# Kernel optimization log

Measured on AMD Instinct MI355X. Metric: run time of the kernel, lower is better.

The kernel has to match this reference:

```python
import jax, jax.numpy as jnp
import numpy as np

HIDDEN = 768
NUM_HEADS = 12
HEAD_SIZE = HIDDEN // NUM_HEADS
LN_EPS = 1e-5


def setup_inputs() -> dict:
    key = jax.random.key(0)
    ks = jax.random.split(key, 10)
    B, S, H = 2, 4096, HIDDEN
    std = 1.0 / np.sqrt(H)
    inp = {
        "hidden_states": jax.random.normal(ks[0], (B, S, H), dtype=jnp.float32),
        "attention_mask": jnp.ones((B, S), dtype=jnp.float32),
        "Wq": jax.random.normal(ks[1], (H, H), dtype=jnp.float32) * std,
        "bq": jnp.zeros((H,), dtype=jnp.float32),
        "Wk": jax.random.normal(ks[2], (H, H), dtype=jnp.float32) * std,
        "bk": jnp.zeros((H,), dtype=jnp.float32),
        "Wv": jax.random.normal(ks[3], (H, H), dtype=jnp.float32) * std,
        "bv": jnp.zeros((H,), dtype=jnp.float32),
        "Wo": jax.random.normal(ks[4], (H, H), dtype=jnp.float32) * std,
        "bo": jnp.zeros((H,), dtype=jnp.float32),
        "ln_gamma": jnp.ones((H,), dtype=jnp.float32),
        "ln_beta": jnp.zeros((H,), dtype=jnp.float32),
    }
    return inp


def _split_heads(x):
    # [B, S, H] -> [B, nH, S, hd]
    B, S, _ = x.shape
    return x.reshape(B, S, NUM_HEADS, HEAD_SIZE).transpose(0, 2, 1, 3)


def reference(hidden_states, attention_mask, Wq, bq, Wk, bk, Wv, bv, Wo, bo, ln_gamma, ln_beta):
    # QKV projections (torch Linear: x @ W.T + b; here W is stored as [in, out])
    q = _split_heads(hidden_states @ Wq + bq)
    k = _split_heads(hidden_states @ Wk + bk)
    v = _split_heads(hidden_states @ Wv + bv)

    scores = jnp.einsum("bhqd,bhkd->bhqk", q, k) / jnp.sqrt(jnp.float32(HEAD_SIZE))
    # additive mask: (1 - mask) * -10000, broadcast over heads and query positions
    scores = scores + (1.0 - attention_mask)[:, None, None, :] * -10000.0
    probs = jax.nn.softmax(scores, axis=-1)  # dropout_prob = 0 -> identity

    ctx = jnp.einsum("bhqk,bhkd->bhqd", probs, v)
    B, _, S, _ = ctx.shape
    ctx = ctx.transpose(0, 2, 1, 3).reshape(B, S, HIDDEN)

    out = ctx @ Wo + bo
    resid = out + hidden_states
    mu = jnp.mean(resid, axis=-1, keepdims=True)
    var = jnp.var(resid, axis=-1, keepdims=True)
    return (resid - mu) * jax.lax.rsqrt(var + LN_EPS) * ln_gamma + ln_beta
```

## Files before the change

### kernel.cpp

```cpp
#include <hip/hip_runtime.h>
#include <hip/hip_bf16.h>

#define HID 768
#define NHEADS 12
#define HDIM 64
#define SEQ 4096
#define BB 2
#define MTOT (BB * SEQ)

typedef __attribute__((ext_vector_type(8))) short bf16x8;
typedef __attribute__((ext_vector_type(16))) float f32x16;

#define LOG2E 1.4426950408889634f

__device__ inline unsigned pack2bf(float a, float b) {
    __hip_bfloat162 h = __float22bfloat162_rn(float2{a, b});
    return *(unsigned*)&h;
}

__global__ __launch_bounds__(256) void cast_x_kernel(
    const float* __restrict__ X, __hip_bfloat16* __restrict__ Xb)
{
    const size_t i = ((size_t)blockIdx.x * 256 + threadIdx.x) * 8;
    const float4 x0 = *(const float4*)(X + i);
    const float4 x1 = *(const float4*)(X + i + 4);
    unsigned u[4];
    u[0] = pack2bf(x0.x, x0.y);
    u[1] = pack2bf(x0.z, x0.w);
    u[2] = pack2bf(x1.x, x1.y);
    u[3] = pack2bf(x1.z, x1.w);
    *(uint4*)(Xb + i) = *(uint4*)u;
}

__global__ __launch_bounds__(256) void pack_w_kernel(
    const float* __restrict__ Wq, const float* __restrict__ Wk,
    const float* __restrict__ Wv, const float* __restrict__ Wo,
    __hip_bfloat16* __restrict__ Wt)
{
    const int z = blockIdx.z;
    const float* __restrict__ W = (z == 0) ? Wq : (z == 1) ? Wk : (z == 2) ? Wv : Wo;
    const int in0  = blockIdx.x * 64;
    const int out0 = blockIdx.y * 64;
    const int t = threadIdx.x;

    __shared__ float T[64][65];
#pragma unroll
    for (int i = 0; i < 4; ++i) {
        const int idx = t + 256 * i;
        const int row = idx >> 4;
        const int c4  = (idx & 15) << 2;
        const float4 v = *(const float4*)(W + (size_t)(in0 + row) * HID + out0 + c4);
        T[row][c4 + 0] = v.x; T[row][c4 + 1] = v.y;
        T[row][c4 + 2] = v.z; T[row][c4 + 3] = v.w;
    }
    __syncthreads();

    const int o  = t >> 2;
    const int cb = (t & 3) << 4;
    __hip_bfloat16 tmp[16];
#pragma unroll
    for (int k = 0; k < 16; ++k)
        tmp[k] = __float2bfloat16(T[cb + k][o]);
    __hip_bfloat16* __restrict__ dst =
        Wt + (size_t)(z * HID + out0 + o) * HID + in0 + cb;
    *(uint4*)(dst)     = *(uint4*)(&tmp[0]);
    *(uint4*)(dst + 8) = *(uint4*)(&tmp[8]);
}

#define GSTAGE(ASB, BSB, BUF, APTR, BPTR, K0) do {                                 \
    _Pragma("unroll")                                                              \
    for (int j_ = 0; j_ < 4; ++j_) {                                               \
        const __hip_bfloat16* ga_ = (APTR) + (size_t)(r0 + 32 * j_) * HID + (K0) + csw; \
        const __hip_bfloat16* gb_ = (BPTR) + (size_t)(r0 + 32 * j_) * HID + (K0) + csw; \
        __builtin_amdgcn_global_load_lds(                                          \
            (const __attribute__((address_space(1))) unsigned*)ga_,                \
            (__attribute__((address_space(3))) unsigned*)(&ASB[BUF][0][0] + (256 * j_ + 64 * w) * 8), 16, 0, 0); \
        __builtin_amdgcn_global_load_lds(                                          \
            (const __attribute__((address_space(1))) unsigned*)gb_,                \
            (__attribute__((address_space(3))) unsigned*)(&BSB[BUF][0][0] + (256 * j_ + 64 * w) * 8), 16, 0, 0); \
    }                                                                              \
} while (0)

#define GTILE(ASB, BSB, BUF) do {                                                  \
    _Pragma("unroll")                                                              \
    for (int kh = 0; kh < 4; ++kh) {                                               \
        const int sc = ((2 * kh + g) ^ (col & 7)) << 3;                            \
        const bf16x8 a0 = *(const bf16x8*)&ASB[BUF][64 * wm + col][sc];            \
        const bf16x8 a1 = *(const bf16x8*)&ASB[BUF][64 * wm + 32 + col][sc];       \
        const bf16x8 b0 = *(const bf16x8*)&BSB[BUF][64 * wn + col][sc];            \
        const bf16x8 b1 = *(const bf16x8*)&BSB[BUF][64 * wn + 32 + col][sc];       \
        acc[0][0] = __builtin_amdgcn_mfma_f32_32x32x16_bf16(a0, b0, acc[0][0], 0, 0, 0); \
        acc[0][1] = __builtin_amdgcn_mfma_f32_32x32x16_bf16(a0, b1, acc[0][1], 0, 0, 0); \
        acc[1][0] = __builtin_amdgcn_mfma_f32_32x32x16_bf16(a1, b0, acc[1][0], 0, 0, 0); \
        acc[1][1] = __builtin_amdgcn_mfma_f32_32x32x16_bf16(a1, b1, acc[1][1], 0, 0, 0); \
    }                                                                              \
} while (0)

__global__ __launch_bounds__(256) void qkv_mfma_kernel(
    const __hip_bfloat16* __restrict__ Xb, const __hip_bfloat16* __restrict__ Wt,
    const float* __restrict__ bq, const float* __restrict__ bk,
    const float* __restrict__ bv,
    __hip_bfloat16* __restrict__ Qo, __hip_bfloat16* __restrict__ Ko,
    __hip_bfloat16* __restrict__ Vo)
{
    const int nblk = blockIdx.x;
    const int z  = nblk / 6;
    const int f0 = (nblk % 6) * 128;
    const int n0 = nblk * 128;
    const int m0 = blockIdx.y * 128;

    const float* __restrict__ bias = (z == 0) ? bq : (z == 1) ? bk : bv;

    const int t    = threadIdx.x;
    const int w    = t >> 6;
    const int lane = t & 63;
    const int col  = lane & 31;
    const int g    = lane >> 5;
    const int wm   = w & 1;
    const int wn   = w >> 1;

    __shared__ __hip_bfloat16 smem[4 * 128 * 64];
    __hip_bfloat16 (*Asb)[128][64] = (__hip_bfloat16(*)[128][64])smem;
    __hip_bfloat16 (*Bsb)[128][64] = (__hip_bfloat16(*)[128][64])(smem + 2 * 128 * 64);

    const int r0  = t >> 3;
    const int csw = (((t & 7) ^ (r0 & 7)) << 3);

    const __hip_bfloat16* __restrict__ Am = Xb + (size_t)m0 * HID;
    const __hip_bfloat16* __restrict__ Bn = Wt + (size_t)n0 * HID;

    f32x16 acc[2][2];
#pragma unroll
    for (int mt = 0; mt < 2; ++mt)
#pragma unroll
        for (int nt = 0; nt < 2; ++nt)
#pragma unroll
            for (int r = 0; r < 16; ++r) acc[mt][nt][r] = 0.f;

    GSTAGE(Asb, Bsb, 0, Am, Bn, 0);
    __syncthreads();
    for (int k0 = 0; k0 < HID; k0 += 128) {
        GSTAGE(Asb, Bsb, 1, Am, Bn, k0 + 64);
        GTILE(Asb, Bsb, 0);
        __syncthreads();
        if (k0 + 128 < HID) GSTAGE(Asb, Bsb, 0, Am, Bn, k0 + 128);
        GTILE(Asb, Bsb, 1);
        __syncthreads();
    }

    if (z < 2) {
        __hip_bfloat16* __restrict__ Out = (z == 0) ? Qo : Ko;
        const int h = (f0 >> 6) + wn;
#pragma unroll
        for (int mt = 0; mt < 2; ++mt)
#pragma unroll
            for (int nt = 0; nt < 2; ++nt) {
                const int d = 32 * nt + col;
                const float bsv = bias[f0 + 64 * wn + d];
#pragma unroll
                for (int r = 0; r < 16; ++r) {
                    const int m = m0 + 64 * wm + 32 * mt + (r & 3) + 8 * (r >> 2) + 4 * g;
                    const int b = m >> 12;
                    const int s = m & (SEQ - 1);
                    Out[(((size_t)(b * NHEADS + h)) * SEQ + s) * HDIM + d] =
                        __float2bfloat16(acc[mt][nt][r] + bsv);
                }
            }
    } else {
        __syncthreads();
        __hip_bfloat16 (*Ts)[136] = (__hip_bfloat16(*)[136])smem;
#pragma unroll
        for (int mt = 0; mt < 2; ++mt)
#pragma unroll
            for (int nt = 0; nt < 2; ++nt) {
                const int nloc = 64 * wn + 32 * nt + col;
                const float bsv = bias[f0 + nloc];
#pragma unroll
                for (int rg = 0; rg < 4; ++rg) {
                    const int mbase = 64 * wm + 32 * mt + 8 * rg + 4 * g;
                    unsigned pu[2];
                    pu[0] = pack2bf(acc[mt][nt][4 * rg + 0] + bsv,
                                    acc[mt][nt][4 * rg + 1] + bsv);
                    pu[1] = pack2bf(acc[mt][nt][4 * rg + 2] + bsv,
                                    acc[mt][nt][4 * rg + 3] + bsv);
                    *(uint2*)&Ts[nloc][mbase] = *(uint2*)pu;
                }
            }
        __syncthreads();
        const int nloc = t >> 1;
        const int half = t & 1;
        const int hh = (f0 >> 6) + (nloc >> 6);
        const int d  = nloc & 63;
        const int bb = m0 >> 12;
        const int s0 = m0 & (SEQ - 1);
        __hip_bfloat16* __restrict__ dst =
            Vo + (((size_t)(bb * NHEADS + hh)) * HDIM + d) * SEQ + s0 + 64 * half;
        const __hip_bfloat16* srcp = &Ts[nloc][64 * half];
#pragma unroll
        for (int j = 0; j < 8; ++j)
            *(uint4*)(dst + 8 * j) = *(const uint4*)(srcp + 8 * j);
    }
}

typedef __attribute__((ext_vector_type(2))) unsigned uswap2;

__global__ __launch_bounds__(256, 3) void attn_kernel(
    const __hip_bfloat16* __restrict__ Qb, const __hip_bfloat16* __restrict__ Kb,
    const __hip_bfloat16* __restrict__ Vt, const float* __restrict__ mask,
    __hip_bfloat16* __restrict__ Op, float* __restrict__ lp)
{
    const int bh = blockIdx.y;
    const int b  = bh / NHEADS;
    const int h  = bh - b * NHEADS;
    const int kspan = SEQ / gridDim.z;
    const int kbeg  = blockIdx.z * kspan;

    const int t    = threadIdx.x;
    const int w    = t >> 6;
    const int lane = t & 63;
    const int col  = lane & 31;
    const int g    = lane >> 5;
    const int qw   = blockIdx.x * 128 + 32 * w;

    __shared__ __hip_bfloat16 Ksb[2][64][64];
    __shared__ __hip_bfloat16 Vsb[2][64][64];
    __shared__ float madd[2048];

    const __hip_bfloat16* __restrict__ Qh = Qb + (size_t)bh * SEQ * HDIM;
    const __hip_bfloat16* __restrict__ Kh = Kb + (size_t)bh * SEQ * HDIM;
    const __hip_bfloat16* __restrict__ Vh = Vt + (size_t)bh * HDIM * SEQ;

    for (int j = t; j < kspan; j += 256)
        madd[j] = (1.0f - mask[b * SEQ + kbeg + j]) * (-10000.0f * LOG2E);

    const int r0  = t >> 3;
    const int csw = (((t & 7) ^ (r0 & 7)) << 3);

#define STAGE(BUF, KT) do {                                                        \
    const __hip_bfloat16* gk0_ = Kh + (size_t)((KT) + r0) * HDIM + csw;            \
    const __hip_bfloat16* gk1_ = Kh + (size_t)((KT) + r0 + 32) * HDIM + csw;       \
    const __hip_bfloat16* gv0_ = Vh + (size_t)r0 * SEQ + (KT) + csw;               \
    const __hip_bfloat16* gv1_ = Vh + (size_t)(r0 + 32) * SEQ + (KT) + csw;        \
    __hip_bfloat16* lk_ = &Ksb[BUF][0][0] + w * 512;                               \
    __hip_bfloat16* lv_ = &Vsb[BUF][0][0] + w * 512;                               \
    __builtin_amdgcn_global_load_lds(                                              \
        (const __attribute__((address_space(1))) unsigned*)gk0_,                   \
        (__attribute__((address_space(3))) unsigned*)lk_, 16, 0, 0);               \
    __builtin_amdgcn_global_load_lds(                                              \
        (const __attribute__((address_space(1))) unsigned*)gk1_,                   \
        (__attribute__((address_space(3))) unsigned*)(lk_ + 2048), 16, 0, 0);      \
    __builtin_amdgcn_global_load_lds(                                              \
        (const __attribute__((address_space(1))) unsigned*)gv0_,                   \
        (__attribute__((address_space(3))) unsigned*)lv_, 16, 0, 0);               \
    __builtin_amdgcn_global_load_lds(                                              \
        (const __attribute__((address_space(1))) unsigned*)gv1_,                   \
        (__attribute__((address_space(3))) unsigned*)(lv_ + 2048), 16, 0, 0);      \
} while (0)

    bf16x8 bq[4];
#pragma unroll
    for (int kh = 0; kh < 4; ++kh)
        bq[kh] = *(const bf16x8*)(Qh + (size_t)(qw + col) * HDIM + 16 * kh + 8 * g);

    f32x16 O[2];
    float lac = 0.f;
#pragma unroll
    for (int dt = 0; dt < 2; ++dt)
#pragma unroll
        for (int r = 0; r < 16; ++r) O[dt][r] = 0.f;

    const float kscale = 0.125f * LOG2E;

#define ATTN_TILE(BUF, KT0) do {                                                   \
    f32x16 St[2];                                                                  \
    _Pragma("unroll")                                                              \
    for (int nt = 0; nt < 2; ++nt)                                                 \
        _Pragma("unroll")                                                          \
        for (int r = 0; r < 16; ++r) St[nt][r] = 0.f;                              \
    _Pragma("unroll")                                                              \
    for (int kh = 0; kh < 4; ++kh) {                                               \
        const int sc = ((2 * kh + g) ^ (col & 7)) << 3;                            \
        const bf16x8 ak0 = *(const bf16x8*)&Ksb[BUF][col][sc];                     \
        const bf16x8 ak1 = *(const bf16x8*)&Ksb[BUF][32 + col][sc];                \
        St[0] = __builtin_amdgcn_mfma_f32_32x32x16_bf16(ak0, bq[kh], St[0], 0, 0, 0); \
        St[1] = __builtin_amdgcn_mfma_f32_32x32x16_bf16(ak1, bq[kh], St[1], 0, 0, 0); \
    }                                                                              \
    unsigned g4x[2][4], g4y[2][4];                                                 \
    _Pragma("unroll")                                                              \
    for (int nt = 0; nt < 2; ++nt) {                                               \
        _Pragma("unroll")                                                          \
        for (int b4 = 0; b4 < 4; ++b4) {                                           \
            const float4 mm = *(const float4*)&madd[(KT0) + 32 * nt + 8 * b4 + 4 * g]; \
            const float p0 = __builtin_amdgcn_exp2f(fmaf(St[nt][4 * b4 + 0], kscale, mm.x)); \
            const float p1 = __builtin_amdgcn_exp2f(fmaf(St[nt][4 * b4 + 1], kscale, mm.y)); \
            const float p2 = __builtin_amdgcn_exp2f(fmaf(St[nt][4 * b4 + 2], kscale, mm.z)); \
            const float p3 = __builtin_amdgcn_exp2f(fmaf(St[nt][4 * b4 + 3], kscale, mm.w)); \
            lac += (p0 + p1) + (p2 + p3);                                          \
            g4x[nt][b4] = pack2bf(p0, p1);                                         \
            g4y[nt][b4] = pack2bf(p2, p3);                                         \
        }                                                                          \
    }                                                                              \
    _Pragma("unroll")                                                              \
    for (int kh = 0; kh < 4; ++kh) {                                               \
        const int nt  = kh >> 1;                                                   \
        const int khl = kh & 1;                                                    \
        union { unsigned u[4]; bf16x8 v; } au;                                     \
        ATTN_PTRANS(au, g4x[nt][2 * khl], g4x[nt][2 * khl + 1],                    \
                        g4y[nt][2 * khl], g4y[nt][2 * khl + 1]);                   \
        const int sc = ((2 * kh + g) ^ (col & 7)) << 3;                            \
        const bf16x8 bv0 = *(const bf16x8*)&Vsb[BUF][col][sc];                     \
        const bf16x8 bv1 = *(const bf16x8*)&Vsb[BUF][32 + col][sc];                \
        O[0] = __builtin_amdgcn_mfma_f32_32x32x16_bf16(au.v, bv0, O[0], 0, 0, 0);  \
        O[1] = __builtin_amdgcn_mfma_f32_32x32x16_bf16(au.v, bv1, O[1], 0, 0, 0);  \
    }                                                                              \
} while (0)

#if __has_builtin(__builtin_amdgcn_permlane32_swap)
#define ATTN_PTRANS(au, lox, hix, loy, hiy) do {                                   \
    uswap2 sx_ = __builtin_amdgcn_permlane32_swap((lox), (hix), false, false);     \
    uswap2 sy_ = __builtin_amdgcn_permlane32_swap((loy), (hiy), false, false);     \
    au.u[0] = sx_[0]; au.u[1] = sy_[0]; au.u[2] = sx_[1]; au.u[3] = sy_[1];        \
} while (0)
#else
#define ATTN_PTRANS(au, lox, hix, loy, hiy) do {                                   \
    const unsigned sxv_ = g ? (lox) : (hix);                                       \
    const unsigned syv_ = g ? (loy) : (hiy);                                       \
    const unsigned rx_ = (unsigned)__shfl_xor((int)sxv_, 32, 64);                  \
    const unsigned ry_ = (unsigned)__shfl_xor((int)syv_, 32, 64);                  \
    if (g) { au.u[0] = rx_;   au.u[1] = ry_;   au.u[2] = (hix); au.u[3] = (hiy); } \
    else   { au.u[0] = (lox); au.u[1] = (loy); au.u[2] = rx_;   au.u[3] = ry_;  }  \
} while (0)
#endif

    STAGE(0, kbeg);
    __syncthreads();

    for (int kt0 = 0; kt0 < kspan; kt0 += 128) {
        STAGE(1, kbeg + kt0 + 64);
        ATTN_TILE(0, kt0);
        __syncthreads();
        if (kt0 + 128 < kspan) STAGE(0, kbeg + kt0 + 128);
        ATTN_TILE(1, kt0 + 64);
        __syncthreads();
    }
#undef STAGE
#undef ATTN_TILE
#undef ATTN_PTRANS

    const size_t opbase = (size_t)blockIdx.z * ((size_t)MTOT * HID);
    {
        const float l = lac + __shfl_xor(lac, 32, 64);
        if (g == 0)
            lp[((size_t)blockIdx.z * (BB * NHEADS) + bh) * SEQ + qw + col] = l;
#pragma unroll
        for (int dt = 0; dt < 2; ++dt)
#pragma unroll
            for (int r = 0; r < 16; ++r) {
                const int q = qw + (r & 3) + 8 * (r >> 2) + 4 * g;
                const int d = 32 * dt + col;
                Op[opbase + ((size_t)b * SEQ + q) * HID + h * HDIM + d] =
                    __float2bfloat16(O[dt][r]);
            }
    }
}

__global__ __launch_bounds__(256) void combine_kernel(
    const __hip_bfloat16* __restrict__ Op, const float* __restrict__ lp,
    __hip_bfloat16* __restrict__ Ctx, int KS)
{
    const size_t i = ((size_t)blockIdx.x * 256 + threadIdx.x) * 8;
    const int n   = (int)(i % HID);
    const int row = (int)(i / HID);
    const int h = n >> 6;
    const int b = row >> 12;
    const int q = row & (SEQ - 1);
    const int bh = b * NHEADS + h;

    float denom = 0.f;
    float o[8] = {};
    for (int kz = 0; kz < KS; ++kz) {
        denom += lp[((size_t)kz * (BB * NHEADS) + bh) * SEQ + q];
        uint4 u = *(const uint4*)(Op + (size_t)kz * ((size_t)MTOT * HID) + i);
        const __hip_bfloat16* e = (const __hip_bfloat16*)&u;
#pragma unroll
        for (int j = 0; j < 8; ++j) o[j] += __bfloat162float(e[j]);
    }
    const float inv = 1.0f / denom;
    unsigned u[4];
#pragma unroll
    for (int j = 0; j < 4; ++j)
        u[j] = pack2bf(o[2 * j] * inv, o[2 * j + 1] * inv);
    *(uint4*)(Ctx + i) = *(uint4*)u;
}

__global__ __launch_bounds__(256) void out_mfma_kernel(
    const __hip_bfloat16* __restrict__ Cb, const __hip_bfloat16* __restrict__ Wto,
    const float* __restrict__ bo, const float* __restrict__ X,
    float* __restrict__ Resid)
{
    const int n0 = blockIdx.x * 128;
    const int m0 = blockIdx.y * 128;

    const int t    = threadIdx.x;
    const int w    = t >> 6;
    const int lane = t & 63;
    const int col  = lane & 31;
    const int g    = lane >> 5;
    const int wm   = w & 1;
    const int wn   = w >> 1;

    __shared__ __hip_bfloat16 smem[4 * 128 * 64];
    __hip_bfloat16 (*Asb)[128][64] = (__hip_bfloat16(*)[128][64])smem;
    __hip_bfloat16 (*Bsb)[128][64] = (__hip_bfloat16(*)[128][64])(smem + 2 * 128 * 64);

    const int r0  = t >> 3;
    const int csw = (((t & 7) ^ (r0 & 7)) << 3);

    const __hip_bfloat16* __restrict__ Am = Cb  + (size_t)m0 * HID;
    const __hip_bfloat16* __restrict__ Bn = Wto + (size_t)n0 * HID;

    f32x16 acc[2][2];
#pragma unroll
    for (int mt = 0; mt < 2; ++mt)
#pragma unroll
        for (int nt = 0; nt < 2; ++nt)
#pragma unroll
            for (int r = 0; r < 16; ++r) acc[mt][nt][r] = 0.f;

    GSTAGE(Asb, Bsb, 0, Am, Bn, 0);
    __syncthreads();
    for (int k0 = 0; k0 < HID; k0 += 128) {
        GSTAGE(Asb, Bsb, 1, Am, Bn, k0 + 64);
        GTILE(Asb, Bsb, 0);
        __syncthreads();
        if (k0 + 128 < HID) GSTAGE(Asb, Bsb, 0, Am, Bn, k0 + 128);
        GTILE(Asb, Bsb, 1);
        __syncthreads();
    }

#pragma unroll
    for (int mt = 0; mt < 2; ++mt)
#pragma unroll
        for (int nt = 0; nt < 2; ++nt) {
            const int n = n0 + 64 * wn + 32 * nt + col;
            const float bsv = bo[n];
#pragma unroll
            for (int r = 0; r < 16; ++r) {
                const int m = m0 + 64 * wm + 32 * mt + (r & 3) + 8 * (r >> 2) + 4 * g;
                Resid[(size_t)m * HID + n] = acc[mt][nt][r] + bsv + X[(size_t)m * HID + n];
            }
        }
}

__global__ __launch_bounds__(256) void ln_kernel(
    const float* __restrict__ Rin, const float* __restrict__ gamma,
    const float* __restrict__ beta, float* __restrict__ Out)
{
    const int row = blockIdx.x;
    const int t   = threadIdx.x;
    const float* __restrict__ x = Rin + (size_t)row * HID;

    const float v0 = x[t];
    const float v1 = x[t + 256];
    const float v2 = x[t + 512];
    float s  = v0 + v1 + v2;
    float s2 = v0 * v0 + v1 * v1 + v2 * v2;
#pragma unroll
    for (int off = 32; off; off >>= 1) {
        s  += __shfl_xor(s,  off, 64);
        s2 += __shfl_xor(s2, off, 64);
    }
    __shared__ float rs[4], rs2[4];
    const int w = t >> 6, lane = t & 63;
    if (lane == 0) { rs[w] = s; rs2[w] = s2; }
    __syncthreads();
    const float tot  = rs[0] + rs[1] + rs[2] + rs[3];
    const float tot2 = rs2[0] + rs2[1] + rs2[2] + rs2[3];
    const float mu   = tot * (1.0f / HID);
    const float var  = tot2 * (1.0f / HID) - mu * mu;
    const float rsig = rsqrtf(var + 1e-5f);

    float* __restrict__ y = Out + (size_t)row * HID;
    y[t]       = (v0 - mu) * rsig * gamma[t]       + beta[t];
    y[t + 256] = (v1 - mu) * rsig * gamma[t + 256] + beta[t + 256];
    y[t + 512] = (v2 - mu) * rsig * gamma[t + 512] + beta[t + 512];
}

extern "C" void kernel_launch(void* const* d_in, const int* in_sizes, int n_in,
                              void* d_out, int out_size, void* d_ws, size_t ws_size,
                              hipStream_t stream)
{
    const float* X     = (const float*)d_in[0];
    const float* mask  = (const float*)d_in[1];
    const float* Wq    = (const float*)d_in[2];
    const float* bq    = (const float*)d_in[3];
    const float* Wk    = (const float*)d_in[4];
    const float* bk    = (const float*)d_in[5];
    const float* Wv    = (const float*)d_in[6];
    const float* bv    = (const float*)d_in[7];
    const float* Wo    = (const float*)d_in[8];
    const float* bo    = (const float*)d_in[9];
    const float* gamma = (const float*)d_in[10];
    const float* beta  = (const float*)d_in[11];
    float* out = (float*)d_out;

    const size_t N = (size_t)MTOT * HID;
    const size_t WTE = (size_t)4 * HID * HID;

    char* p = (char*)d_ws;
    __hip_bfloat16* Xb  = (__hip_bfloat16*)p;  p += 2 * N;
    __hip_bfloat16* Wt  = (__hip_bfloat16*)p;  p += 2 * WTE;
    __hip_bfloat16* Qw  = (__hip_bfloat16*)p;  p += 2 * N;
    __hip_bfloat16* Kw  = (__hip_bfloat16*)p;  p += 2 * N;
    __hip_bfloat16* Vtw = (__hip_bfloat16*)p;  p += 2 * N;
    char* opb = p;
    const size_t fixed = (size_t)(opb - (char*)d_ws);

    const size_t lpsz4 = 4 * (size_t)(BB * NHEADS) * SEQ * sizeof(float);
    const int KS = (ws_size >= fixed + 4 * 2 * N + lpsz4) ? 4 : 2;

    __hip_bfloat16* Op  = (__hip_bfloat16*)opb;
    float* lpt = (float*)(opb + (size_t)KS * 2 * N);
    __hip_bfloat16* Ctxb = Xb;
    float* Rd = (float*)Kw;

    cast_x_kernel<<<(int)(N / 2048), 256, 0, stream>>>(X, Xb);
    pack_w_kernel<<<dim3(12, 12, 4), 256, 0, stream>>>(Wq, Wk, Wv, Wo, Wt);
    qkv_mfma_kernel<<<dim3(18, MTOT / 128), 256, 0, stream>>>(
        Xb, Wt, bq, bk, bv, Qw, Kw, Vtw);
    attn_kernel<<<dim3(SEQ / 128, BB * NHEADS, KS), 256, 0, stream>>>(
        Qw, Kw, Vtw, mask, Op, lpt);
    combine_kernel<<<(int)(N / 2048), 256, 0, stream>>>(Op, lpt, Ctxb, KS);
    out_mfma_kernel<<<dim3(6, MTOT / 128), 256, 0, stream>>>(
        Ctxb, Wt + (size_t)2304 * HID, bo, X, Rd);
    ln_kernel<<<MTOT, 256, 0, stream>>>(Rd, gamma, beta, out);
}
```

Before: 332.5 us.

## Drop split-K attention and combine kernel; normalize inside attention epilogue

Removes the key-dimension split (grid z) so each attention block processes the full sequence and normalizes its output directly. This eliminates the combine kernel and the partial Op/lp buffers, cutting their global memory traffic. It also pre-loads the mask bias into the MFMA accumulator, scaled so that kscale times the value gives the same bias. In exchange the grid drops to 768 blocks, which lowers parallelism, and the larger shared mask array raises LDS use per block and may reduce occupancy.

```diff
diff --git a/kernel.cpp b/kernel.cpp
--- a/kernel.cpp
+++ b/kernel.cpp
@@ -207,13 +207,11 @@
 __global__ __launch_bounds__(256, 3) void attn_kernel(
     const __hip_bfloat16* __restrict__ Qb, const __hip_bfloat16* __restrict__ Kb,
     const __hip_bfloat16* __restrict__ Vt, const float* __restrict__ mask,
-    __hip_bfloat16* __restrict__ Op, float* __restrict__ lp)
+    __hip_bfloat16* __restrict__ Ctx)
 {
     const int bh = blockIdx.y;
     const int b  = bh / NHEADS;
     const int h  = bh - b * NHEADS;
-    const int kspan = SEQ / gridDim.z;
-    const int kbeg  = blockIdx.z * kspan;
 
     const int t    = threadIdx.x;
     const int w    = t >> 6;
@@ -224,14 +222,15 @@
 
     __shared__ __hip_bfloat16 Ksb[2][64][64];
     __shared__ __hip_bfloat16 Vsb[2][64][64];
-    __shared__ float madd[2048];
+    __shared__ float madd[SEQ];
+    __shared__ float ls[4][32];
 
     const __hip_bfloat16* __restrict__ Qh = Qb + (size_t)bh * SEQ * HDIM;
     const __hip_bfloat16* __restrict__ Kh = Kb + (size_t)bh * SEQ * HDIM;
     const __hip_bfloat16* __restrict__ Vh = Vt + (size_t)bh * HDIM * SEQ;
 
-    for (int j = t; j < kspan; j += 256)
-        madd[j] = (1.0f - mask[b * SEQ + kbeg + j]) * (-10000.0f * LOG2E);
+    for (int j = t; j < SEQ; j += 256)
+        madd[j] = (1.0f - mask[b * SEQ + j]) * (-80000.0f);
 
     const int r0  = t >> 3;
     const int csw = (((t & 7) ^ (r0 & 7)) << 3);
@@ -276,7 +275,11 @@
     _Pragma("unroll")                                                              \
     for (int nt = 0; nt < 2; ++nt)                                                 \
         _Pragma("unroll")                                                          \
-        for (int r = 0; r < 16; ++r) St[nt][r] = 0.f;                              \
+        for (int b4 = 0; b4 < 4; ++b4) {                                           \
+            const float4 mm = *(const float4*)&madd[(KT0) + 32 * nt + 8 * b4 + 4 * g]; \
+            St[nt][4 * b4 + 0] = mm.x; St[nt][4 * b4 + 1] = mm.y;                  \
+            St[nt][4 * b4 + 2] = mm.z; St[nt][4 * b4 + 3] = mm.w;                  \
+        }                                                                          \
     _Pragma("unroll")                                                              \
     for (int kh = 0; kh < 4; ++kh) {                                               \
         const int sc = ((2 * kh + g) ^ (col & 7)) << 3;                            \
@@ -290,11 +293,10 @@
     for (int nt = 0; nt < 2; ++nt) {                                               \
         _Pragma("unroll")                                                          \
         for (int b4 = 0; b4 < 4; ++b4) {                                           \
-            const float4 mm = *(const float4*)&madd[(KT0) + 32 * nt + 8 * b4 + 4 * g]; \
-            const float p0 = __builtin_amdgcn_exp2f(fmaf(St[nt][4 * b4 + 0], kscale, mm.x)); \
-            const float p1 = __builtin_amdgcn_exp2f(fmaf(St[nt][4 * b4 + 1], kscale, mm.y)); \
-            const float p2 = __builtin_amdgcn_exp2f(fmaf(St[nt][4 * b4 + 2], kscale, mm.z)); \
-            const float p3 = __builtin_amdgcn_exp2f(fmaf(St[nt][4 * b4 + 3], kscale, mm.w)); \
+            const float p0 = __builtin_amdgcn_exp2f(St[nt][4 * b4 + 0] * kscale);  \
+            const float p1 = __builtin_amdgcn_exp2f(St[nt][4 * b4 + 1] * kscale);  \
+            const float p2 = __builtin_amdgcn_exp2f(St[nt][4 * b4 + 2] * kscale);  \
+            const float p3 = __builtin_amdgcn_exp2f(St[nt][4 * b4 + 3] * kscale);  \
             lac += (p0 + p1) + (p2 + p3);                                          \
             g4x[nt][b4] = pack2bf(p0, p1);                                         \
             g4y[nt][b4] = pack2bf(p2, p3);                                         \
@@ -332,14 +334,14 @@
 } while (0)
 #endif
 
-    STAGE(0, kbeg);
+    STAGE(0, 0);
     __syncthreads();
 
-    for (int kt0 = 0; kt0 < kspan; kt0 += 128) {
-        STAGE(1, kbeg + kt0 + 64);
+    for (int kt0 = 0; kt0 < SEQ; kt0 += 128) {
+        STAGE(1, kt0 + 64);
         ATTN_TILE(0, kt0);
         __syncthreads();
-        if (kt0 + 128 < kspan) STAGE(0, kbeg + kt0 + 128);
+        if (kt0 + 128 < SEQ) STAGE(0, kt0 + 128);
         ATTN_TILE(1, kt0 + 64);
         __syncthreads();
     }
@@ -347,50 +349,22 @@
 #undef ATTN_TILE
 #undef ATTN_PTRANS
 
-    const size_t opbase = (size_t)blockIdx.z * ((size_t)MTOT * HID);
     {
         const float l = lac + __shfl_xor(lac, 32, 64);
-        if (g == 0)
-            lp[((size_t)blockIdx.z * (BB * NHEADS) + bh) * SEQ + qw + col] = l;
-#pragma unroll
-        for (int dt = 0; dt < 2; ++dt)
-#pragma unroll
-            for (int r = 0; r < 16; ++r) {
-                const int q = qw + (r & 3) + 8 * (r >> 2) + 4 * g;
+        if (g == 0) ls[w][col] = 1.0f / l;
+#pragma unroll
+        for (int r = 0; r < 16; ++r) {
+            const int qloc = (r & 3) + 8 * (r >> 2) + 4 * g;
+            const float inv = ls[w][qloc];
+            const int q = qw + qloc;
+#pragma unroll
+            for (int dt = 0; dt < 2; ++dt) {
                 const int d = 32 * dt + col;
-                Op[opbase + ((size_t)b * SEQ + q) * HID + h * HDIM + d] =
-                    __float2bfloat16(O[dt][r]);
+                Ctx[((size_t)b * SEQ + q) * HID + h * HDIM + d] =
+                    __float2bfloat16(O[dt][r] * inv);
             }
-    }
-}
-
-__global__ __launch_bounds__(256) void combine_kernel(
-    const __hip_bfloat16* __restrict__ Op, const float* __restrict__ lp,
-    __hip_bfloat16* __restrict__ Ctx, int KS)
-{
-    const size_t i = ((size_t)blockIdx.x * 256 + threadIdx.x) * 8;
-    const int n   = (int)(i % HID);
-    const int row = (int)(i / HID);
-    const int h = n >> 6;
-    const int b = row >> 12;
-    const int q = row & (SEQ - 1);
-    const int bh = b * NHEADS + h;
-
-    float denom = 0.f;
-    float o[8] = {};
-    for (int kz = 0; kz < KS; ++kz) {
-        denom += lp[((size_t)kz * (BB * NHEADS) + bh) * SEQ + q];
-        uint4 u = *(const uint4*)(Op + (size_t)kz * ((size_t)MTOT * HID) + i);
-        const __hip_bfloat16* e = (const __hip_bfloat16*)&u;
-#pragma unroll
-        for (int j = 0; j < 8; ++j) o[j] += __bfloat162float(e[j]);
-    }
-    const float inv = 1.0f / denom;
-    unsigned u[4];
-#pragma unroll
-    for (int j = 0; j < 4; ++j)
-        u[j] = pack2bf(o[2 * j] * inv, o[2 * j + 1] * inv);
-    *(uint4*)(Ctx + i) = *(uint4*)u;
+        }
+    }
 }
 
 __global__ __launch_bounds__(256) void out_mfma_kernel(
@@ -513,14 +487,7 @@
     __hip_bfloat16* Qw  = (__hip_bfloat16*)p;  p += 2 * N;
     __hip_bfloat16* Kw  = (__hip_bfloat16*)p;  p += 2 * N;
     __hip_bfloat16* Vtw = (__hip_bfloat16*)p;  p += 2 * N;
-    char* opb = p;
-    const size_t fixed = (size_t)(opb - (char*)d_ws);
-
-    const size_t lpsz4 = 4 * (size_t)(BB * NHEADS) * SEQ * sizeof(float);
-    const int KS = (ws_size >= fixed + 4 * 2 * N + lpsz4) ? 4 : 2;
-
-    __hip_bfloat16* Op  = (__hip_bfloat16*)opb;
-    float* lpt = (float*)(opb + (size_t)KS * 2 * N);
+
     __hip_bfloat16* Ctxb = Xb;
     float* Rd = (float*)Kw;
 
@@ -528,9 +495,8 @@
     pack_w_kernel<<<dim3(12, 12, 4), 256, 0, stream>>>(Wq, Wk, Wv, Wo, Wt);
     qkv_mfma_kernel<<<dim3(18, MTOT / 128), 256, 0, stream>>>(
         Xb, Wt, bq, bk, bv, Qw, Kw, Vtw);
-    attn_kernel<<<dim3(SEQ / 128, BB * NHEADS, KS), 256, 0, stream>>>(
-        Qw, Kw, Vtw, mask, Op, lpt);
-    combine_kernel<<<(int)(N / 2048), 256, 0, stream>>>(Op, lpt, Ctxb, KS);
+    attn_kernel<<<dim3(SEQ / 128, BB * NHEADS), 256, 0, stream>>>(
+        Qw, Kw, Vtw, mask, Ctxb);
     out_mfma_kernel<<<dim3(6, MTOT / 128), 256, 0, stream>>>(
         Ctxb, Wt + (size_t)2304 * HID, bo, X, Rd);
     ln_kernel<<<MTOT, 256, 0, stream>>>(Rd, gamma, beta, out);
```

New measurement: 324.1 us. -2.5%, faster.
